# Optimization experiments

Hardware: AMD Instinct MI355X
Metric: run time of the kernel (lower is better)

The kernel has to match this reference:

```python
import jax, jax.numpy as jnp
import numpy as np

B, TT, TP, TO = 8, 128, 256, 512
V, D, H, L = 1024, 1024, 16, 12
FF = 4 * D
DH = D // H
EPS = 1e-5


def _pe(t, d):
    # sinusoidal PE: concat(sin(omega*t), cos(omega*t)), omega = exp(-ln(1e4)*i/(d/2))
    half = d // 2
    omega = jnp.exp(-jnp.log(10000.0) * jnp.arange(half, dtype=jnp.float32) / half)
    ang = jnp.arange(t, dtype=jnp.float32)[:, None] * omega[None, :]  # (t, d/2)
    return jnp.concatenate([jnp.sin(ang), jnp.cos(ang)], axis=-1)  # (t, d)


def _ln(x, g, b):
    mu = x.mean(axis=-1, keepdims=True)
    var = ((x - mu) ** 2).mean(axis=-1, keepdims=True)
    return (x - mu) / jnp.sqrt(var + EPS) * g + b


def _forward(text_ids, prompt_ids, output_ids, text_tab, prompt_tab, output_tab, sep,
             ln1_g, ln1_b, qkv_w, out_w, out_b, ln2_g, ln2_b,
             ff1_w, ff1_b, ff2_w, ff2_b, fc_w, fc_b):
    emb = lambda ids, tab: tab[ids] + _pe(ids.shape[1], D)[None]
    sep_tok = jnp.broadcast_to(sep, (B, 1, D))
    # join: [text, sep, prompt, sep, output]
    x = jnp.concatenate([emb(text_ids, text_tab), sep_tok,
                         emb(prompt_ids, prompt_tab), sep_tok,
                         emb(output_ids, output_tab)], axis=1)  # (B, T, D)
    T = x.shape[1]
    causal = jnp.tril(jnp.ones((T, T), dtype=bool))  # (T, T)
    scale = DH ** -0.5
    neg = -jnp.finfo(x.dtype).max
    for l in range(L):
        # attention block (prenorm residual); uniform lengths -> mask m is all ones
        h = _ln(x, ln1_g[l], ln1_b[l])
        qkv = h @ qkv_w[l]  # (B, T, 3D)
        q, k, v = jnp.split(qkv, 3, axis=-1)
        q = q.reshape(B, T, H, DH)
        k = k.reshape(B, T, H, DH)
        v = v.reshape(B, T, H, DH)
        e = jnp.einsum('bihd,bjhd->bijh', q, k) * scale
        e = jnp.where(causal[None, :, :, None], e, neg)
        a = jax.nn.softmax(e, axis=2)
        o = jnp.einsum('bijh,bjhd->bihd', a, v).reshape(B, T, D)
        x = x + o @ out_w[l] + out_b[l]
        # ffn block (prenorm residual), exact GELU as torch nn.GELU default
        h2 = _ln(x, ln2_g[l], ln2_b[l])
        ff = jax.nn.gelu(h2 @ ff1_w[l] + ff1_b[l], approximate=False) @ ff2_w[l] + ff2_b[l]
        x = x + ff
    h = x @ fc_w + fc_b  # (B, T, V)
    return h[:, -1, :]  # logits of last position, (B, V)


def setup_inputs() -> dict:
    key = jax.random.key(0)
    ks = iter(jax.random.split(key, 32))
    s = 0.02
    inp = {
        'text_ids': jax.random.randint(next(ks), (B, TT), 0, V),
        'prompt_ids': jax.random.randint(next(ks), (B, TP), 0, V),
        'output_ids': jax.random.randint(next(ks), (B, TO), 0, V),
        'text_tab': jax.random.normal(next(ks), (V, D), jnp.float32) * s,
        'prompt_tab': jax.random.normal(next(ks), (V, D), jnp.float32) * s,
        'output_tab': jax.random.normal(next(ks), (V, D), jnp.float32) * s,
        'sep': jax.random.normal(next(ks), (D,), jnp.float32),
        'ln1_g': jnp.ones((L, D), jnp.float32),
        'ln1_b': jnp.zeros((L, D), jnp.float32),
        'qkv_w': jax.random.normal(next(ks), (L, D, 3 * D), jnp.float32) * s,
        'out_w': jax.random.normal(next(ks), (L, D, D), jnp.float32) * s,
        'out_b': jnp.zeros((L, D), jnp.float32),
        'ln2_g': jnp.ones((L, D), jnp.float32),
        'ln2_b': jnp.zeros((L, D), jnp.float32),
        'ff1_w': jax.random.normal(next(ks), (L, D, FF), jnp.float32) * s,
        'ff1_b': jnp.zeros((L, FF), jnp.float32),
        'ff2_w': jax.random.normal(next(ks), (L, FF, D), jnp.float32) * s,
        'ff2_b': jnp.zeros((L, D), jnp.float32),
        'fc_w': jax.random.normal(next(ks), (D, V), jnp.float32) * s,
        'fc_b': jnp.zeros((V,), jnp.float32),
    }
    return inp


def reference(text_ids, prompt_ids, output_ids, text_tab, prompt_tab, output_tab, sep,
              ln1_g, ln1_b, qkv_w, out_w, out_b, ln2_g, ln2_b,
              ff1_w, ff1_b, ff2_w, ff2_b, fc_w, fc_b):
    return _forward(text_ids, prompt_ids, output_ids, text_tab, prompt_tab, output_tab, sep,
                    ln1_g, ln1_b, qkv_w, out_w, out_b, ln2_g, ln2_b,
                    ff1_w, ff1_b, ff2_w, ff2_b, fc_w, fc_b)
```

## Files before the change

### kernel.cpp

```cpp
#include <hip/hip_runtime.h>
#include <hip/hip_bf16.h>
#include <math.h>

#define Bn 8
#define Tn 898
#define Dn 1024
#define Hn 16
#define DHn 64
#define Ln 12
#define FFn 4096
#define Vn 1024
#define BT (Bn*Tn)

typedef short bf16x8 __attribute__((ext_vector_type(8)));
typedef float f32x4 __attribute__((ext_vector_type(4)));

__device__ __forceinline__ ushort f2bf(float f) {
    union { float f; unsigned u; } c; c.f = f;
    unsigned r = c.u + 0x7fffu + ((c.u >> 16) & 1u);
    return (ushort)(r >> 16);
}

__device__ __forceinline__ void glds16(const void* g, void* l) {
    __builtin_amdgcn_global_load_lds(
        (const __attribute__((address_space(1))) unsigned int*)g,
        (__attribute__((address_space(3))) unsigned int*)l, 16, 0, 0);
}

#define BARRIER() __builtin_amdgcn_s_barrier()
#define VMCNT0() asm volatile("s_waitcnt vmcnt(0)" ::: "memory")

__global__ __launch_bounds__(256) void transpose_cast_kernel(
    const float* __restrict__ in, ushort* __restrict__ out,
    int K, int N, size_t in_ls, size_t out_ls)
{
    __shared__ ushort t[64][68];
    const float* inp = in + (size_t)blockIdx.z * in_ls;
    ushort* outp = out + (size_t)blockIdx.z * out_ls;
    int n0 = blockIdx.x * 64, k0 = blockIdx.y * 64;
    int tx = threadIdx.x & 63, ty = threadIdx.x >> 6;
    #pragma unroll
    for (int p = 0; p < 16; p++) {
        int kl = p * 4 + ty;
        t[tx][kl] = f2bf(inp[(size_t)(k0 + kl) * N + n0 + tx]);
    }
    __syncthreads();
    int tx4 = threadIdx.x & 15, ty4 = threadIdx.x >> 4;
    #pragma unroll
    for (int p = 0; p < 4; p++) {
        int nl = p * 16 + ty4;
        ushort4 v;
        v.x = t[nl][4*tx4]; v.y = t[nl][4*tx4+1]; v.z = t[nl][4*tx4+2]; v.w = t[nl][4*tx4+3];
        *(ushort4*)&outp[(size_t)(n0 + nl) * K + k0 + 4*tx4] = v;
    }
}

__global__ __launch_bounds__(256) void embed_kernel(
    const int* __restrict__ tids, const int* __restrict__ pids, const int* __restrict__ oids,
    const float* __restrict__ ttab, const float* __restrict__ ptab, const float* __restrict__ otab,
    const float* __restrict__ sep, float* __restrict__ x)
{
    int bp = blockIdx.x;
    int b = bp / Tn, pos = bp - b * Tn;
    int d0 = threadIdx.x * 4;
    float4 r;
    if (pos == 128 || pos == 385) {
        r = *(const float4*)(sep + d0);
    } else {
        int t; int id; const float* tab;
        if (pos < 128)      { t = pos;       id = tids[b*128 + t]; tab = ttab; }
        else if (pos < 385) { t = pos - 129; id = pids[b*256 + t]; tab = ptab; }
        else                { t = pos - 386; id = oids[b*512 + t]; tab = otab; }
        float4 e = *(const float4*)(tab + (size_t)id * Dn + d0);
        float pe[4];
        #pragma unroll
        for (int i = 0; i < 4; i++) {
            int d = d0 + i;
            int ii = d & 511;
            float omega = expf(-9.210340371976184f * (float)ii * (1.0f/512.0f));
            float ang = (float)t * omega;
            pe[i] = (d < 512) ? sinf(ang) : cosf(ang);
        }
        r.x = e.x + pe[0]; r.y = e.y + pe[1]; r.z = e.z + pe[2]; r.w = e.w + pe[3];
    }
    *(float4*)(x + (size_t)bp * Dn + d0) = r;
}

__global__ __launch_bounds__(256) void ln_kernel(
    const float* __restrict__ x, const float* __restrict__ g, const float* __restrict__ bt,
    ushort* __restrict__ out)
{
    int row = blockIdx.x * 4 + (threadIdx.x >> 6);
    int lane = threadIdx.x & 63;
    const float4* xr = (const float4*)(x + (size_t)row * Dn);
    float4 v[4];
    float s = 0.f;
    #pragma unroll
    for (int i = 0; i < 4; i++) {
        v[i] = xr[lane + 64 * i];
        s += v[i].x + v[i].y + v[i].z + v[i].w;
    }
    #pragma unroll
    for (int o = 32; o; o >>= 1) s += __shfl_xor(s, o);
    float mu = s * (1.0f / Dn);
    float s2 = 0.f;
    #pragma unroll
    for (int i = 0; i < 4; i++) {
        v[i].x -= mu; v[i].y -= mu; v[i].z -= mu; v[i].w -= mu;
        s2 += v[i].x*v[i].x + v[i].y*v[i].y + v[i].z*v[i].z + v[i].w*v[i].w;
    }
    #pragma unroll
    for (int o = 32; o; o >>= 1) s2 += __shfl_xor(s2, o);
    float rstd = rsqrtf(s2 * (1.0f / Dn) + 1e-5f);
    ushort4* orow = (ushort4*)(out + (size_t)row * Dn);
    #pragma unroll
    for (int i = 0; i < 4; i++) {
        float4 gg = ((const float4*)g)[lane + 64 * i];
        float4 bb = ((const float4*)bt)[lane + 64 * i];
        ushort4 o4;
        o4.x = f2bf(v[i].x * rstd * gg.x + bb.x);
        o4.y = f2bf(v[i].y * rstd * gg.y + bb.y);
        o4.z = f2bf(v[i].z * rstd * gg.z + bb.z);
        o4.w = f2bf(v[i].w * rstd * gg.w + bb.w);
        orow[lane + 64 * i] = o4;
    }
}

__device__ __forceinline__ void raster(int nb, int bid, int nx, int S, int nmt,
                                       int& mt, int& ntt)
{
    int qq = nb >> 3, rr8 = nb & 7;
    int xcd = bid & 7, idx = bid >> 3;
    int wg = (xcd < rr8 ? xcd * (qq + 1) : rr8 * (qq + 1) + (xcd - rr8) * qq) + idx;
    int fullb = nmt / S, per = S * nx;
    if (wg < fullb * per) {
        int band = wg / per, r2 = wg - band * per;
        ntt = r2 / S; mt = band * S + (r2 - ntt * S);
    } else {
        int r2 = wg - fullb * per, bh = nmt - fullb * S;
        ntt = r2 / bh; mt = fullb * S + (r2 - ntt * bh);
    }
}

template<int BM, int BN, int MODE>
__global__ __launch_bounds__(256, 4) void gemmk(
    const ushort* __restrict__ A, const ushort* __restrict__ Bw,
    const float* __restrict__ bias, const float* __restrict__ resid,
    void* __restrict__ Cout, int M, int N, int K, int nx, int S)
{
    constexpr int MI = BM / 32, NI = BN / 32;
    constexpr int UA = BM / 64, UB = BN / 64;
    __shared__ ushort sA[2][BM * 32];
    __shared__ ushort sB[2][BN * 32];

    int tid = threadIdx.x, lane = tid & 63, wv = tid >> 6;
    int wm = wv >> 1, wn = wv & 1;
    int l16 = lane & 15, lhi = lane >> 4;

    int mt, ntt;
    raster(gridDim.x, blockIdx.x, nx, S, (M + BM - 1) / BM, mt, ntt);
    int m0 = mt * BM, n0 = ntt * BN;

    f32x4 acc[MI][NI];
    #pragma unroll
    for (int i = 0; i < MI; i++)
        #pragma unroll
        for (int j = 0; j < NI; j++) acc[i][j] = (f32x4){0.f, 0.f, 0.f, 0.f};

    const size_t K2 = (size_t)K * 2;
    int srow = lane >> 2;
    int schk = ((lane & 3) ^ ((lane >> 3) & 3)) * 16;
    const char* Ap[UA];
    const char* Bp[UB];
    #pragma unroll
    for (int i = 0; i < UA; i++)
        Ap[i] = (const char*)A + (size_t)(m0 + (wv + 4 * i) * 16 + srow) * K2 + schk;
    #pragma unroll
    for (int i = 0; i < UB; i++)
        Bp[i] = (const char*)Bw + (size_t)(n0 + (wv + 4 * i) * 16 + srow) * K2 + schk;

    auto stage = [&](int buf) {
        #pragma unroll
        for (int i = 0; i < UA; i++) {
            glds16(Ap[i], (char*)sA[buf] + (wv + 4 * i) * 1024);
            Ap[i] += 64;
        }
        #pragma unroll
        for (int i = 0; i < UB; i++) {
            glds16(Bp[i], (char*)sB[buf] + (wv + 4 * i) * 1024);
            Bp[i] += 64;
        }
    };

    const int sc = (lhi ^ ((l16 >> 1) & 3)) * 8;
    auto compute = [&](int buf) {
        bf16x8 af[MI], bf[NI];
        #pragma unroll
        for (int mi = 0; mi < MI; mi++)
            af[mi] = *(const bf16x8*)&sA[buf][(wm * (16 * MI) + mi * 16 + l16) * 32 + sc];
        #pragma unroll
        for (int ni = 0; ni < NI; ni++)
            bf[ni] = *(const bf16x8*)&sB[buf][(wn * (16 * NI) + ni * 16 + l16) * 32 + sc];
        #pragma unroll
        for (int mi = 0; mi < MI; mi++)
            #pragma unroll
            for (int ni = 0; ni < NI; ni++)
                acc[mi][ni] = __builtin_amdgcn_mfma_f32_16x16x32_bf16(af[mi], bf[ni], acc[mi][ni], 0, 0, 0);
    };

    int ntile = K >> 5;
    stage(0);
    VMCNT0();
    BARRIER();
    int cur = 0;
    for (int t = 0; t < ntile; ++t) {
        if (t + 1 < ntile) stage(cur ^ 1);
        compute(cur);
        VMCNT0();
        BARRIER();
        cur ^= 1;
    }

    #pragma unroll
    for (int mi = 0; mi < MI; mi++) {
        int rl = wm * (16 * MI) + mi * 16 + lhi * 4;
        #pragma unroll
        for (int ni = 0; ni < NI; ni++) {
            int gcol = n0 + wn * (16 * NI) + ni * 16 + l16;
            float bs = (MODE == 0) ? 0.0f : bias[gcol];
            #pragma unroll
            for (int j = 0; j < 4; j++) {
                int grow = m0 + rl + j;
                if (grow >= M) continue;
                float v = acc[mi][ni][j] + bs;
                if (MODE == 1) {
                    float rv = resid[(size_t)grow * N + gcol];
                    ((float*)Cout)[(size_t)grow * N + gcol] = rv + v;
                } else if (MODE == 2) {
                    float u = v * (1.5957691216f + 0.0713548163f * v * v);
                    float g = v / (1.0f + __expf(-u));
                    ((ushort*)Cout)[(size_t)grow * N + gcol] = f2bf(g);
                } else {
                    ((ushort*)Cout)[(size_t)grow * N + gcol] = f2bf(v);
                }
            }
        }
    }
}

template<int MODE>
__global__ __launch_bounds__(512, 2) void gemm256(
    const ushort* __restrict__ A, const ushort* __restrict__ Bw,
    const float* __restrict__ bias, void* __restrict__ Cout,
    int M, int N, int K, int nx, int S)
{
    __shared__ ushort sAB[2][512 * 64];

    int tid = threadIdx.x, lane = tid & 63, wv = tid >> 6;
    int wm = wv >> 2, wn = wv & 3;
    int l16 = lane & 15, lhi = lane >> 4;

    int mt, ntt;
    raster(gridDim.x, blockIdx.x, nx, S, (M + 255) >> 8, mt, ntt);
    int m0 = mt * 256, n0 = ntt * 256;

    f32x4 acc[8][4];
    #pragma unroll
    for (int i = 0; i < 8; i++)
        #pragma unroll
        for (int j = 0; j < 4; j++) acc[i][j] = (f32x4){0.f, 0.f, 0.f, 0.f};

    const size_t K2 = (size_t)K * 2;
    int srow = lane >> 3;
    int schk = ((lane & 7) ^ srow) * 16;
    const char* Pp[8];
    #pragma unroll
    for (int i = 0; i < 8; i++) {
        int u = wv + 8 * i;
        int grow = (u < 32) ? (m0 + u * 8 + srow) : 0;
        const char* base = (const char*)A;
        if (u >= 32) { grow = n0 + (u - 32) * 8 + srow; base = (const char*)Bw; }
        Pp[i] = base + (size_t)grow * K2 + schk;
    }

    auto stage = [&](int buf) {
        #pragma unroll
        for (int i = 0; i < 8; i++) {
            glds16(Pp[i], (char*)sAB[buf] + (wv + 8 * i) * 1024);
            Pp[i] += 128;
        }
    };

    auto compute = [&](int buf) {
        const ushort* Sb = sAB[buf];
        #pragma unroll
        for (int ks = 0; ks < 2; ks++) {
            const int sc = (((ks << 2) | lhi) ^ (l16 & 7)) * 8;
            bf16x8 af[8], bf[4];
            #pragma unroll
            for (int mi = 0; mi < 8; mi++)
                af[mi] = *(const bf16x8*)&Sb[(wm * 128 + mi * 16 + l16) * 64 + sc];
            #pragma unroll
            for (int ni = 0; ni < 4; ni++)
                bf[ni] = *(const bf16x8*)&Sb[(256 + wn * 64 + ni * 16 + l16) * 64 + sc];
            #pragma unroll
            for (int mi = 0; mi < 8; mi++)
                #pragma unroll
                for (int ni = 0; ni < 4; ni++)
                    acc[mi][ni] = __builtin_amdgcn_mfma_f32_16x16x32_bf16(af[mi], bf[ni], acc[mi][ni], 0, 0, 0);
        }
    };

    int ntile = K >> 6;
    stage(0);
    VMCNT0();
    BARRIER();
    int cur = 0;
    for (int t = 0; t < ntile; ++t) {
        if (t + 1 < ntile) stage(cur ^ 1);
        compute(cur);
        VMCNT0();
        BARRIER();
        cur ^= 1;
    }

    #pragma unroll
    for (int mi = 0; mi < 8; mi++) {
        int rl = wm * 128 + mi * 16 + lhi * 4;
        #pragma unroll
        for (int ni = 0; ni < 4; ni++) {
            int gcol = n0 + wn * 64 + ni * 16 + l16;
            float bs = (MODE == 0) ? 0.0f : bias[gcol];
            #pragma unroll
            for (int j = 0; j < 4; j++) {
                int grow = m0 + rl + j;
                if (grow >= M) continue;
                float v = acc[mi][ni][j] + bs;
                if (MODE == 2) {
                    float u = v * (1.5957691216f + 0.0713548163f * v * v);
                    float g = v / (1.0f + __expf(-u));
                    ((ushort*)Cout)[(size_t)grow * N + gcol] = f2bf(g);
                } else {
                    ((ushort*)Cout)[(size_t)grow * N + gcol] = f2bf(v);
                }
            }
        }
    }
}

__global__ __launch_bounds__(256) void attn_kernel(
    const ushort* __restrict__ qkv, ushort* __restrict__ out)
{
    __shared__ ushort Ksm[64 * 72];
    __shared__ ushort Vsm[64 * 72];
    __shared__ ushort Psm[4][16 * 72];
    int qt = blockIdx.x, b = blockIdx.y, h = blockIdx.z;
    int tid = threadIdx.x, lane = tid & 63, wave = tid >> 6;
    int l16 = lane & 15, lhi = lane >> 4;

    int qrow = qt*64 + wave*16 + l16;
    bf16x8 qf0 = {}, qf1 = {};
    if (qrow < Tn) {
        const ushort* qp = qkv + (size_t)(b*Tn + qrow) * 3072 + h*64 + lhi*8;
        qf0 = *(const bf16x8*)qp;
        qf1 = *(const bf16x8*)(qp + 32);
    }

    f32x4 o[4];
    #pragma unroll
    for (int i = 0; i < 4; i++) o[i] = (f32x4){0.f,0.f,0.f,0.f};
    float mrun[4] = {-1e30f,-1e30f,-1e30f,-1e30f};
    float sume[4] = {0.f,0.f,0.f,0.f};

    int kr = tid >> 2, cc = (tid & 3) * 16;
    const ushort* kvbase = qkv + (size_t)(b*Tn) * 3072 + h*64 + cc;
    int qg = qt*64 + wave*16 + lhi*4;

    for (int jt = 0; jt <= qt; jt++) {
        int kvr = jt*64 + kr;
        uint4 k0 = make_uint4(0,0,0,0), k1 = k0, v0 = k0, v1 = k0;
        if (kvr < Tn) {
            const ushort* p = kvbase + (size_t)kvr * 3072;
            k0 = *(const uint4*)(p + 1024);
            k1 = *(const uint4*)(p + 1024 + 8);
            v0 = *(const uint4*)(p + 2048);
            v1 = *(const uint4*)(p + 2048 + 8);
        }
        __syncthreads();
        *(uint4*)&Ksm[kr * 72 + cc] = k0;
        *(uint4*)&Ksm[kr * 72 + cc + 8] = k1;
        {
            ushort vv[16];
            *(uint4*)&vv[0] = v0; *(uint4*)&vv[8] = v1;
            #pragma unroll
            for (int i = 0; i < 16; i++) Vsm[(cc + i) * 72 + kr] = vv[i];
        }
        __syncthreads();

        f32x4 s[4];
        #pragma unroll
        for (int ni = 0; ni < 4; ni++) {
            s[ni] = (f32x4){0.f,0.f,0.f,0.f};
            bf16x8 kf0 = *(const bf16x8*)&Ksm[(ni*16 + l16) * 72 + lhi*8];
            bf16x8 kf1 = *(const bf16x8*)&Ksm[(ni*16 + l16) * 72 + lhi*8 + 32];
            s[ni] = __builtin_amdgcn_mfma_f32_16x16x32_bf16(qf0, kf0, s[ni], 0, 0, 0);
            s[ni] = __builtin_amdgcn_mfma_f32_16x16x32_bf16(qf1, kf1, s[ni], 0, 0, 0);
        }

        float pv[4][4];
        #pragma unroll
        for (int j = 0; j < 4; j++) {
            int qgj = qg + j;
            float mx = -1e30f;
            #pragma unroll
            for (int ni = 0; ni < 4; ni++) {
                int kvg = jt*64 + ni*16 + l16;
                float e = (kvg <= qgj && kvg < Tn) ? s[ni][j] * 0.125f : -1e30f;
                pv[ni][j] = e;
                mx = fmaxf(mx, e);
            }
            #pragma unroll
            for (int m = 1; m < 16; m <<= 1) mx = fmaxf(mx, __shfl_xor(mx, m));
            float mnew = fmaxf(mrun[j], mx);
            float fac = expf(mrun[j] - mnew);
            mrun[j] = mnew;
            float rs = 0.f;
            #pragma unroll
            for (int ni = 0; ni < 4; ni++) { pv[ni][j] = expf(pv[ni][j] - mnew); rs += pv[ni][j]; }
            #pragma unroll
            for (int m = 1; m < 16; m <<= 1) rs += __shfl_xor(rs, m);
            sume[j] = sume[j] * fac + rs;
            #pragma unroll
            for (int di = 0; di < 4; di++) o[di][j] *= fac;
        }

        #pragma unroll
        for (int j = 0; j < 4; j++)
            #pragma unroll
            for (int ni = 0; ni < 4; ni++)
                Psm[wave][(lhi*4 + j) * 72 + ni*16 + l16] = f2bf(pv[ni][j]);
        __syncthreads();

        bf16x8 pf0 = *(const bf16x8*)&Psm[wave][l16 * 72 + lhi*8];
        bf16x8 pf1 = *(const bf16x8*)&Psm[wave][l16 * 72 + lhi*8 + 32];
        #pragma unroll
        for (int di = 0; di < 4; di++) {
            bf16x8 vf0 = *(const bf16x8*)&Vsm[(di*16 + l16) * 72 + lhi*8];
            bf16x8 vf1 = *(const bf16x8*)&Vsm[(di*16 + l16) * 72 + lhi*8 + 32];
            o[di] = __builtin_amdgcn_mfma_f32_16x16x32_bf16(pf0, vf0, o[di], 0, 0, 0);
            o[di] = __builtin_amdgcn_mfma_f32_16x16x32_bf16(pf1, vf1, o[di], 0, 0, 0);
        }
    }

    #pragma unroll
    for (int j = 0; j < 4; j++) {
        int qgj = qg + j;
        if (qgj >= Tn) continue;
        float inv = 1.0f / sume[j];
        #pragma unroll
        for (int di = 0; di < 4; di++)
            out[(size_t)(b*Tn + qgj) * Dn + h*64 + di*16 + l16] = f2bf(o[di][j] * inv);
    }
}

__global__ __launch_bounds__(256) void fc_kernel(
    const float* __restrict__ x, const float* __restrict__ w,
    const float* __restrict__ bias, float* __restrict__ out)
{
    __shared__ float xs[Dn];
    int b = blockIdx.y;
    int v = blockIdx.x * 256 + threadIdx.x;
    float4 t = ((const float4*)(x + (size_t)(b*Tn + Tn - 1) * Dn))[threadIdx.x];
    ((float4*)xs)[threadIdx.x] = t;
    __syncthreads();
    float acc = bias[v];
    for (int d = 0; d < Dn; d++)
        acc = fmaf(xs[d], w[(size_t)d * Vn + v], acc);
    out[(size_t)b * Vn + v] = acc;
}

extern "C" void kernel_launch(void* const* d_in, const int* in_sizes, int n_in,
                              void* d_out, int out_size, void* d_ws, size_t ws_size,
                              hipStream_t stream)
{
    const int*   text_ids  = (const int*)d_in[0];
    const int*   prompt_ids= (const int*)d_in[1];
    const int*   output_ids= (const int*)d_in[2];
    const float* text_tab  = (const float*)d_in[3];
    const float* prompt_tab= (const float*)d_in[4];
    const float* output_tab= (const float*)d_in[5];
    const float* sep       = (const float*)d_in[6];
    const float* ln1_g     = (const float*)d_in[7];
    const float* ln1_b     = (const float*)d_in[8];
    const float* qkv_w     = (const float*)d_in[9];
    const float* out_w     = (const float*)d_in[10];
    const float* out_b     = (const float*)d_in[11];
    const float* ln2_g     = (const float*)d_in[12];
    const float* ln2_b     = (const float*)d_in[13];
    const float* ff1_w     = (const float*)d_in[14];
    const float* ff1_b     = (const float*)d_in[15];
    const float* ff2_w     = (const float*)d_in[16];
    const float* ff2_b     = (const float*)d_in[17];
    const float* fc_w      = (const float*)d_in[18];
    const float* fc_b      = (const float*)d_in[19];

    char* ws = (char*)d_ws;
    float*  x    = (float*)(ws);
    ushort* h    = (ushort*)(ws + 29425664);
    ushort* qkv  = (ushort*)(ws + 44630016);
    ushort* attn = (ushort*)(ws + 90243072);
    ushort* ff1o = (ushort*)(ws + 105447424);
    ushort* wT   = (ushort*)(ws + 166264832);

    const size_t L_STRIDE = 12582912;
    const size_t OFF_QKV = 0, OFF_OUT = 3145728, OFF_FF1 = 4194304, OFF_FF2 = 8388608;
    const size_t upfront_need = 166264832ULL + 2ULL * L_STRIDE * Ln;
    const bool upfront = ws_size >= upfront_need;

    if (upfront) {
        transpose_cast_kernel<<<dim3(48,16,Ln), 256, 0, stream>>>(qkv_w, wT + OFF_QKV, Dn, 3*Dn, (size_t)Dn*3*Dn, L_STRIDE);
        transpose_cast_kernel<<<dim3(16,16,Ln), 256, 0, stream>>>(out_w, wT + OFF_OUT, Dn, Dn,   (size_t)Dn*Dn,   L_STRIDE);
        transpose_cast_kernel<<<dim3(64,16,Ln), 256, 0, stream>>>(ff1_w, wT + OFF_FF1, Dn, FFn,  (size_t)Dn*FFn,  L_STRIDE);
        transpose_cast_kernel<<<dim3(16,64,Ln), 256, 0, stream>>>(ff2_w, wT + OFF_FF2, FFn, Dn,  (size_t)FFn*Dn,  L_STRIDE);
    }

    embed_kernel<<<BT, 256, 0, stream>>>(text_ids, prompt_ids, output_ids,
                                         text_tab, prompt_tab, output_tab, sep, x);

    for (int l = 0; l < Ln; l++) {
        ushort* wb = upfront ? (wT + (size_t)l * L_STRIDE) : wT;
        if (!upfront) {
            transpose_cast_kernel<<<dim3(48,16,1), 256, 0, stream>>>(qkv_w + (size_t)l*Dn*3*Dn, wb + OFF_QKV, Dn, 3*Dn, 0, 0);
            transpose_cast_kernel<<<dim3(16,16,1), 256, 0, stream>>>(out_w + (size_t)l*Dn*Dn,   wb + OFF_OUT, Dn, Dn,   0, 0);
            transpose_cast_kernel<<<dim3(64,16,1), 256, 0, stream>>>(ff1_w + (size_t)l*Dn*FFn,  wb + OFF_FF1, Dn, FFn,  0, 0);
            transpose_cast_kernel<<<dim3(16,64,1), 256, 0, stream>>>(ff2_w + (size_t)l*FFn*Dn,  wb + OFF_FF2, FFn, Dn,  0, 0);
        }
        ln_kernel<<<BT/4, 256, 0, stream>>>(x, ln1_g + l*Dn, ln1_b + l*Dn, h);
        gemm256<0><<<29*12, 512, 0, stream>>>(
            h, wb + OFF_QKV, nullptr, qkv, BT, 3*Dn, Dn, 12, 4);
        attn_kernel<<<dim3(15, Bn, Hn), 256, 0, stream>>>(qkv, attn);
        gemmk<64,128,1><<<113*8, 256, 0, stream>>>(
            attn, wb + OFF_OUT, out_b + l*Dn, x, x, BT, Dn, Dn, 8, 4);
        ln_kernel<<<BT/4, 256, 0, stream>>>(x, ln2_g + l*Dn, ln2_b + l*Dn, h);
        gemm256<2><<<29*16, 512, 0, stream>>>(
            h, wb + OFF_FF1, ff1_b + l*FFn, ff1o, BT, FFn, Dn, 16, 4);
        gemmk<64,128,1><<<113*8, 256, 0, stream>>>(
            ff1o, wb + OFF_FF2, ff2_b + l*Dn, x, x, BT, Dn, FFn, 8, 6);
    }

    fc_kernel<<<dim3(Vn/256, Bn), 256, 0, stream>>>(x, fc_w, fc_b, (float*)d_out);
}
```

Before: 5.190 ms.

## Rewrite 256x256 GEMM as 8-phase ping-pong schedule with split LDS halves

Replaces the double-buffered 256x256 GEMM with an 8-phase schedule. LDS is split into A/B halves per buffer, and loads of individual halves are interleaved with MFMA quadrants. Partial vmcnt waits, barriers and s_setprio raise MFMA priority so global->LDS staging overlaps compute. It also adds a separate leading-dimension argument to the smaller GEMM and changes the FF2 raster group size. The extra barriers per tile add sync overhead, and correctness depends on the vmcnt(6) counting matching the issue order.

Measured after the change: 5.172 ms. About the same (-0.3%).

```diff
diff --git a/kernel.cpp b/kernel.cpp
--- a/kernel.cpp
+++ b/kernel.cpp
@@ -28,7 +28,9 @@
 }
 
 #define BARRIER() __builtin_amdgcn_s_barrier()
+#define SETPRIO(p) __builtin_amdgcn_s_setprio(p)
 #define VMCNT0() asm volatile("s_waitcnt vmcnt(0)" ::: "memory")
+#define VMCNT6() asm volatile("s_waitcnt vmcnt(6)" ::: "memory")
 
 __global__ __launch_bounds__(256) void transpose_cast_kernel(
     const float* __restrict__ in, ushort* __restrict__ out,
@@ -146,7 +148,7 @@
 __global__ __launch_bounds__(256, 4) void gemmk(
     const ushort* __restrict__ A, const ushort* __restrict__ Bw,
     const float* __restrict__ bias, const float* __restrict__ resid,
-    void* __restrict__ Cout, int M, int N, int K, int nx, int S)
+    void* __restrict__ Cout, int M, int N, int K, int Kld, int nx, int S)
 {
     constexpr int MI = BM / 32, NI = BN / 32;
     constexpr int UA = BM / 64, UB = BN / 64;
@@ -167,7 +169,7 @@
         #pragma unroll
         for (int j = 0; j < NI; j++) acc[i][j] = (f32x4){0.f, 0.f, 0.f, 0.f};
 
-    const size_t K2 = (size_t)K * 2;
+    const size_t K2 = (size_t)Kld * 2;
     int srow = lane >> 2;
     int schk = ((lane & 3) ^ ((lane >> 3) & 3)) * 16;
     const char* Ap[UA];
@@ -227,7 +229,7 @@
         #pragma unroll
         for (int ni = 0; ni < NI; ni++) {
             int gcol = n0 + wn * (16 * NI) + ni * 16 + l16;
-            float bs = (MODE == 0) ? 0.0f : bias[gcol];
+            float bs = (MODE == 1 || MODE == 2) ? bias[gcol] : 0.0f;
             #pragma unroll
             for (int j = 0; j < 4; j++) {
                 int grow = m0 + rl + j;
@@ -249,12 +251,12 @@
 }
 
 template<int MODE>
-__global__ __launch_bounds__(512, 2) void gemm256(
+__global__ __launch_bounds__(512, 2) void gemm8p(
     const ushort* __restrict__ A, const ushort* __restrict__ Bw,
     const float* __restrict__ bias, void* __restrict__ Cout,
     int M, int N, int K, int nx, int S)
 {
-    __shared__ ushort sAB[2][512 * 64];
+    __shared__ ushort lds[2][2][2][128 * 64];
 
     int tid = threadIdx.x, lane = tid & 63, wv = tid >> 6;
     int wm = wv >> 2, wn = wv & 3;
@@ -273,69 +275,117 @@
     const size_t K2 = (size_t)K * 2;
     int srow = lane >> 3;
     int schk = ((lane & 7) ^ srow) * 16;
-    const char* Pp[8];
-    #pragma unroll
-    for (int i = 0; i < 8; i++) {
-        int u = wv + 8 * i;
-        int grow = (u < 32) ? (m0 + u * 8 + srow) : 0;
-        const char* base = (const char*)A;
-        if (u >= 32) { grow = n0 + (u - 32) * 8 + srow; base = (const char*)Bw; }
-        Pp[i] = base + (size_t)grow * K2 + schk;
-    }
-
-    auto stage = [&](int buf) {
-        #pragma unroll
-        for (int i = 0; i < 8; i++) {
-            glds16(Pp[i], (char*)sAB[buf] + (wv + 8 * i) * 1024);
-            Pp[i] += 128;
+    const char* Sp[4][2];
+    #pragma unroll
+    for (int j = 0; j < 2; j++) {
+        int r = (wv * 2 + j) * 8 + srow;
+        Sp[0][j] = (const char*)A  + (size_t)(m0 + r)       * K2 + schk;
+        Sp[1][j] = (const char*)A  + (size_t)(m0 + 128 + r) * K2 + schk;
+        Sp[2][j] = (const char*)Bw + (size_t)(n0 + r)       * K2 + schk;
+        Sp[3][j] = (const char*)Bw + (size_t)(n0 + 128 + r) * K2 + schk;
+    }
+
+    auto stageH = [&](int hid, int buf) {
+        #pragma unroll
+        for (int j = 0; j < 2; j++) {
+            glds16(Sp[hid][j], (char*)&lds[buf][hid >> 1][hid & 1][0] + (wv * 2 + j) * 1024);
+            Sp[hid][j] += 128;
         }
     };
 
-    auto compute = [&](int buf) {
-        const ushort* Sb = sAB[buf];
-        #pragma unroll
-        for (int ks = 0; ks < 2; ks++) {
-            const int sc = (((ks << 2) | lhi) ^ (l16 & 7)) * 8;
-            bf16x8 af[8], bf[4];
-            #pragma unroll
-            for (int mi = 0; mi < 8; mi++)
-                af[mi] = *(const bf16x8*)&Sb[(wm * 128 + mi * 16 + l16) * 64 + sc];
-            #pragma unroll
-            for (int ni = 0; ni < 4; ni++)
-                bf[ni] = *(const bf16x8*)&Sb[(256 + wn * 64 + ni * 16 + l16) * 64 + sc];
-            #pragma unroll
-            for (int mi = 0; mi < 8; mi++)
+    bf16x8 afr[4][2], bfr0[2][2], bfr1[2][2];
+    const int bhalf = wn >> 1, brow0 = (wn & 1) * 64;
+
+    auto LDA = [&](int buf, int mh) {
+        #pragma unroll
+        for (int mi = 0; mi < 4; mi++) {
+            int row = mh * 64 + mi * 16 + l16;
+            #pragma unroll
+            for (int ks = 0; ks < 2; ks++) {
+                int sw = (((ks << 2) | lhi) ^ (l16 & 7)) * 8;
+                afr[mi][ks] = *(const bf16x8*)&lds[buf][0][wm][row * 64 + sw];
+            }
+        }
+    };
+    auto LDB = [&](bf16x8 (&b)[2][2], int buf, int nh) {
+        #pragma unroll
+        for (int ni = 0; ni < 2; ni++) {
+            int row = brow0 + nh * 32 + ni * 16 + l16;
+            #pragma unroll
+            for (int ks = 0; ks < 2; ks++) {
+                int sw = (((ks << 2) | lhi) ^ (l16 & 7)) * 8;
+                b[ni][ks] = *(const bf16x8*)&lds[buf][1][bhalf][row * 64 + sw];
+            }
+        }
+    };
+    auto MM = [&](int mh, int nh, bf16x8 (&b)[2][2]) {
+        #pragma unroll
+        for (int ks = 0; ks < 2; ks++)
+            #pragma unroll
+            for (int mi = 0; mi < 4; mi++)
                 #pragma unroll
-                for (int ni = 0; ni < 4; ni++)
-                    acc[mi][ni] = __builtin_amdgcn_mfma_f32_16x16x32_bf16(af[mi], bf[ni], acc[mi][ni], 0, 0, 0);
-        }
+                for (int ni = 0; ni < 2; ni++)
+                    acc[mh*4+mi][nh*2+ni] = __builtin_amdgcn_mfma_f32_16x16x32_bf16(
+                        afr[mi][ks], b[ni][ks], acc[mh*4+mi][nh*2+ni], 0, 0, 0);
     };
 
     int ntile = K >> 6;
-    stage(0);
-    VMCNT0();
+    stageH(0,0); stageH(1,0); stageH(2,0); stageH(3,0);
+    stageH(2,1); stageH(3,1); stageH(0,1); stageH(1,1);
+    VMCNT6();
     BARRIER();
-    int cur = 0;
-    for (int t = 0; t < ntile; ++t) {
-        if (t + 1 < ntile) stage(cur ^ 1);
-        compute(cur);
-        VMCNT0();
-        BARRIER();
-        cur ^= 1;
-    }
-
-    #pragma unroll
-    for (int mi = 0; mi < 8; mi++) {
-        int rl = wm * 128 + mi * 16 + lhi * 4;
-        #pragma unroll
-        for (int ni = 0; ni < 4; ni++) {
-            int gcol = n0 + wn * 64 + ni * 16 + l16;
-            float bs = (MODE == 0) ? 0.0f : bias[gcol];
+
+    for (int t = 0; t < ntile; t += 2) {
+        const bool st2 = (t + 2) < ntile;
+        const bool st3 = (t + 3) < ntile;
+        LDA(0, 0); LDB(bfr0, 0, 0);
+        BARRIER();
+        SETPRIO(1); MM(0, 0, bfr0); SETPRIO(0);
+        BARRIER();
+        LDB(bfr1, 0, 1);
+        BARRIER();
+        SETPRIO(1); MM(0, 1, bfr1); SETPRIO(0);
+        BARRIER();
+        LDA(0, 1);
+        if (st2) stageH(2, 0);
+        BARRIER();
+        SETPRIO(1); MM(1, 1, bfr1); SETPRIO(0);
+        BARRIER();
+        if (st2) { stageH(3, 0); stageH(0, 0); stageH(1, 0); }
+        SETPRIO(1); MM(1, 0, bfr0); SETPRIO(0);
+        if (st2) { VMCNT6(); } else { VMCNT0(); }
+        BARRIER();
+        LDA(1, 0); LDB(bfr0, 1, 0);
+        BARRIER();
+        SETPRIO(1); MM(0, 0, bfr0); SETPRIO(0);
+        BARRIER();
+        LDB(bfr1, 1, 1);
+        BARRIER();
+        SETPRIO(1); MM(0, 1, bfr1); SETPRIO(0);
+        BARRIER();
+        LDA(1, 1);
+        if (st3) stageH(2, 1);
+        BARRIER();
+        SETPRIO(1); MM(1, 1, bfr1); SETPRIO(0);
+        BARRIER();
+        if (st3) { stageH(3, 1); stageH(0, 1); stageH(1, 1); }
+        SETPRIO(1); MM(1, 0, bfr0); SETPRIO(0);
+        if (st3) { VMCNT6(); } else { VMCNT0(); }
+        BARRIER();
+    }
+
+    #pragma unroll
+    for (int mf = 0; mf < 8; mf++) {
+        int rb = m0 + wm * 128 + (mf >> 2) * 64 + (mf & 3) * 16 + lhi * 4;
+        #pragma unroll
+        for (int nf = 0; nf < 4; nf++) {
+            int gcol = n0 + wn * 64 + (nf >> 1) * 32 + (nf & 1) * 16 + l16;
+            float bs = (MODE == 2) ? bias[gcol] : 0.0f;
             #pragma unroll
             for (int j = 0; j < 4; j++) {
-                int grow = m0 + rl + j;
+                int grow = rb + j;
                 if (grow >= M) continue;
-                float v = acc[mi][ni][j] + bs;
+                float v = acc[mf][nf][j] + bs;
                 if (MODE == 2) {
                     float u = v * (1.5957691216f + 0.0713548163f * v * v);
                     float g = v / (1.0f + __expf(-u));
@@ -536,16 +586,16 @@
             transpose_cast_kernel<<<dim3(16,64,1), 256, 0, stream>>>(ff2_w + (size_t)l*FFn*Dn,  wb + OFF_FF2, FFn, Dn,  0, 0);
         }
         ln_kernel<<<BT/4, 256, 0, stream>>>(x, ln1_g + l*Dn, ln1_b + l*Dn, h);
-        gemm256<0><<<29*12, 512, 0, stream>>>(
+        gemm8p<0><<<29*12, 512, 0, stream>>>(
             h, wb + OFF_QKV, nullptr, qkv, BT, 3*Dn, Dn, 12, 4);
         attn_kernel<<<dim3(15, Bn, Hn), 256, 0, stream>>>(qkv, attn);
         gemmk<64,128,1><<<113*8, 256, 0, stream>>>(
-            attn, wb + OFF_OUT, out_b + l*Dn, x, x, BT, Dn, Dn, 8, 4);
+            attn, wb + OFF_OUT, out_b + l*Dn, x, x, BT, Dn, Dn, Dn, 8, 4);
         ln_kernel<<<BT/4, 256, 0, stream>>>(x, ln2_g + l*Dn, ln2_b + l*Dn, h);
-        gemm256<2><<<29*16, 512, 0, stream>>>(
+        gemm8p<2><<<29*16, 512, 0, stream>>>(
             h, wb + OFF_FF1, ff1_b + l*FFn, ff1o, BT, FFn, Dn, 16, 4);
         gemmk<64,128,1><<<113*8, 256, 0, stream>>>(
-            ff1o, wb + OFF_FF2, ff2_b + l*Dn, x, x, BT, Dn, FFn, 8, 6);
+            ff1o, wb + OFF_FF2, ff2_b + l*Dn, x, x, BT, Dn, FFn, FFn, 8, 4);
     }
 
     fc_kernel<<<dim3(Vn/256, Bn), 256, 0, stream>>>(x, fc_w, fc_b, (float*)d_out);
```
